# Kernel optimization log

Measured on AMD Instinct MI355X. Metric: run time of the kernel, lower is better.

## Reference

```python
import jax, jax.numpy as jnp
import numpy as np
import math

HIDDEN = 2048
NUM_HEADS = 16
HEAD_SIZE = HIDDEN // NUM_HEADS
BATCH = 2
SEQ = 2048


def setup_inputs() -> dict:
    key = jax.random.key(0)
    k_x, k_wq, k_bq, k_wo, k_bo = jax.random.split(key, 5)
    scale_in = 1.0 / math.sqrt(HIDDEN)
    return {
        "x": jax.random.normal(k_x, (BATCH, SEQ, HIDDEN), dtype=jnp.float32),
        # torch Linear stored as W[out,in]; we keep the jax-friendly transpose [in,out]
        "Wqkv": jax.random.normal(k_wq, (HIDDEN, 3 * HIDDEN), dtype=jnp.float32) * scale_in,
        "bqkv": jax.random.normal(k_bq, (3 * HIDDEN,), dtype=jnp.float32) * 0.01,
        "Wo": jax.random.normal(k_wo, (HIDDEN, HIDDEN), dtype=jnp.float32) * scale_in,
        "bo": jax.random.normal(k_bo, (HIDDEN,), dtype=jnp.float32) * 0.01,
    }


def reference(x, Wqkv, bqkv, Wo, bo):
    b, s, _ = x.shape
    # fused QKV projection; channel layout is (three, num_heads, head_size)
    kqv = x @ Wqkv + bqkv                      # [b, s, 3*hidden]
    kqv = kqv.reshape(b, s, 3, NUM_HEADS, HEAD_SIZE)
    q = kqv[:, :, 0]                           # [b, s, n, h]
    k = kqv[:, :, 1]
    v = kqv[:, :, 2]
    # scores[b, n, s_key, t_query] = K_s . Q_t, scaled
    scores = jnp.einsum('bsnh,btnh->bnst', k, q) / math.sqrt(HEAD_SIZE)
    # faithful to original: keep upper triangle (key <= query), masked entries are exactly -10000
    ones = jnp.ones_like(scores)
    scores = jnp.triu(scores) + (-10000.0) * jnp.tril(ones, k=-1)
    attn = jax.nn.softmax(scores, axis=2)      # softmax over key dim
    out = jnp.einsum('bnkq,bknh->bqnh', attn, v)  # [b, s, n, h]
    out = out.reshape(b, s, NUM_HEADS * HEAD_SIZE)
    return out @ Wo + bo
```

## Files before the change

kernel.cpp:

```cpp
#include <hip/hip_runtime.h>
#include <hip/hip_bf16.h>

typedef __hip_bfloat16 bf16;
typedef __attribute__((ext_vector_type(8))) short short8;
typedef __attribute__((ext_vector_type(8))) unsigned short ushort8;
typedef __attribute__((ext_vector_type(4))) float floatx4;

#define BATCH 2
#define S_LEN 2048
#define NHEAD 16
#define HD 128
#define HIDDEN 2048
#define QSCALE 0.12754435f
#define FOFF 12.0f

static __device__ __forceinline__ unsigned short f2bf(float f) {
    union { float f; unsigned int u; } c; c.f = f;
    unsigned int u = c.u;
    unsigned int rounded = u + 0x7FFF + ((u >> 16) & 1);
    return (unsigned short)(rounded >> 16);
}

__global__ __launch_bounds__(256) void cast_f32_bf16(const float* __restrict__ src,
                                                     bf16* __restrict__ dst) {
    int i = (blockIdx.x * 256 + threadIdx.x) * 8;
    float4 a = *(const float4*)&src[i];
    float4 b = *(const float4*)&src[i + 4];
    ushort8 o;
    o[0] = f2bf(a.x); o[1] = f2bf(a.y); o[2] = f2bf(a.z); o[3] = f2bf(a.w);
    o[4] = f2bf(b.x); o[5] = f2bf(b.y); o[6] = f2bf(b.z); o[7] = f2bf(b.w);
    *(ushort8*)&dst[i] = o;
}

__global__ __launch_bounds__(256) void cast_transpose(const float* __restrict__ src,
                                                      bf16* __restrict__ dst,
                                                      int R, int C) {
    __shared__ unsigned short t[32][33];
    int tx = threadIdx.x & 31, ty = threadIdx.x >> 5;
    int c0 = blockIdx.x * 32, r0 = blockIdx.y * 32;
#pragma unroll
    for (int i = 0; i < 4; i++) {
        int r = r0 + ty + i * 8;
        t[ty + i * 8][tx] = f2bf(src[(size_t)r * C + c0 + tx]);
    }
    __syncthreads();
#pragma unroll
    for (int i = 0; i < 4; i++) {
        int cc = c0 + ty + i * 8;
        ((unsigned short*)dst)[(size_t)cc * R + r0 + tx] = t[tx][ty + i * 8];
    }
}

#define GK 2048
#define NT 32

#define STGA(s, h)                                                              \
    __builtin_amdgcn_global_load_lds(                                           \
        (const __attribute__((address_space(1))) void*)(pA + (size_t)((h) * 64) * GK + (s) * 64), \
        (__attribute__((address_space(3))) void*)(lA + ((s) & 1) * 32768 + (h) * 8192 + ldst),    \
        16, 0, 0)
#define STGB(s, h)                                                              \
    __builtin_amdgcn_global_load_lds(                                           \
        (const __attribute__((address_space(1))) void*)(pB + (size_t)((h) * 64) * GK + (s) * 64), \
        (__attribute__((address_space(3))) void*)(lB + ((s) & 1) * 16384 + (h) * 8192 + ldst),    \
        16, 0, 0)

#define LDA(i, ks) (*(const short8*)(Ab + ((((wm * 64 + (i) * 16 + lr) << 7) + (ks) * 64 + quad * 16) ^ axor)))
#define LDB(j, ks) (*(const short8*)(Bb + ((((wn * 64 + (j) * 16 + lr) << 7) + (ks) * 64 + quad * 16) ^ axor)))

#define PH8(IOFF, BF, JOFF)                                                     \
    __builtin_amdgcn_s_setprio(1);                                              \
    _Pragma("unroll")                                                           \
    for (int ks = 0; ks < 2; ks++)                                              \
        _Pragma("unroll")                                                       \
        for (int ii = 0; ii < 2; ii++)                                          \
            _Pragma("unroll")                                                   \
            for (int jj = 0; jj < 2; jj++)                                      \
                acc[(IOFF) + ii][(JOFF) + jj] = __builtin_amdgcn_mfma_f32_16x16x32_bf16( \
                    aF[ii][ks], BF[jj][ks], acc[(IOFF) + ii][(JOFF) + jj], 0, 0, 0); \
    __builtin_amdgcn_s_setprio(0);

#define BAR __builtin_amdgcn_s_barrier()
#define LGKM0 asm volatile("s_waitcnt lgkmcnt(0)" ::: "memory")

template <int EPI>
__global__ __launch_bounds__(512, 2) void gemm256(const bf16* __restrict__ A,
                                                  const bf16* __restrict__ Bt,
                                                  const float* __restrict__ bias,
                                                  bf16* __restrict__ Qb,
                                                  bf16* __restrict__ Kb,
                                                  bf16* __restrict__ Vt,
                                                  float* __restrict__ Cout,
                                                  int ntN) {
    __shared__ __align__(16) bf16 Asm[2][256 * 64];
    __shared__ __align__(16) bf16 Bsm[2][128 * 64];

    int tid = threadIdx.x;
    int wave = tid >> 6, lane = tid & 63;
    int quad = lane >> 4, lr = lane & 15;
    int wm = wave >> 1, wn = wave & 1;
    int axor = (lr & 7) << 4;

    int nwg = gridDim.x;
    int cpx = nwg >> 3;
    int bid = blockIdx.x;
    int swz = (bid & 7) * cpx + (bid >> 3);
    int mt = swz / ntN, nt = swz - mt * ntN;
    int m0 = mt * 256, n0 = nt * 128;

    int srow = wave * 8 + (lane >> 3);
    int scol = ((lane & 7) ^ ((lane >> 3) & 7)) * 8;
    const bf16* pA = A + (size_t)(m0 + srow) * GK + scol;
    const bf16* pB = Bt + (size_t)(n0 + srow) * GK + scol;
    char* lA = (char*)&Asm[0][0];
    char* lB = (char*)&Bsm[0][0];
    int ldst = wave * 1024;

    const floatx4 fzero = {0.f, 0.f, 0.f, 0.f};
    floatx4 acc[4][4];
#pragma unroll
    for (int i = 0; i < 4; i++)
#pragma unroll
        for (int j = 0; j < 4; j++) acc[i][j] = fzero;

    short8 aF[2][2], b0F[2][2], b1F[2][2];

    STGB(0, 0); STGB(0, 1); STGA(0, 0); STGA(0, 1); STGA(0, 2); STGA(0, 3);
    STGB(1, 0); STGB(1, 1); STGA(1, 0); STGA(1, 1); STGA(1, 2); STGA(1, 3);
    asm volatile("s_waitcnt vmcnt(6)" ::: "memory");
    BAR;

    for (int t = 0; t < NT; ++t) {
        const char* Ab = lA + (t & 1) * 32768;
        const char* Bb = lB + (t & 1) * 16384;

#pragma unroll
        for (int ii = 0; ii < 2; ii++) { aF[ii][0] = LDA(ii, 0); aF[ii][1] = LDA(ii, 1); }
#pragma unroll
        for (int jj = 0; jj < 2; jj++) { b0F[jj][0] = LDB(jj, 0); b0F[jj][1] = LDB(jj, 1); }
        BAR; LGKM0;
        PH8(0, b0F, 0)
        BAR;

#pragma unroll
        for (int jj = 0; jj < 2; jj++) { b1F[jj][0] = LDB(jj + 2, 0); b1F[jj][1] = LDB(jj + 2, 1); }
        BAR; LGKM0;
        PH8(0, b1F, 2)
        BAR;

#pragma unroll
        for (int ii = 0; ii < 2; ii++) { aF[ii][0] = LDA(ii + 2, 0); aF[ii][1] = LDA(ii + 2, 1); }
        if (t + 2 < NT) { STGB(t + 2, 0); STGB(t + 2, 1); }
        BAR; LGKM0;
        PH8(2, b1F, 2)
        BAR;

        if (t + 2 < NT) {
            STGA(t + 2, 0); STGA(t + 2, 1); STGA(t + 2, 2); STGA(t + 2, 3);
            asm volatile("s_waitcnt vmcnt(6)" ::: "memory");
        } else {
            asm volatile("s_waitcnt vmcnt(0)" ::: "memory");
        }
        BAR;
        PH8(2, b0F, 0)
        BAR;
    }

    if (EPI == 0) {
#pragma unroll
        for (int i = 0; i < 4; i++) {
#pragma unroll
            for (int j = 0; j < 4; j++) {
                int gcn = n0 + wn * 64 + j * 16 + lr;
                float bv = bias[gcn];
                int tsel = gcn >> 11, hh = (gcn >> 7) & 15, d = gcn & 127;
#pragma unroll
                for (int reg = 0; reg < 4; reg++) {
                    int gm = m0 + wm * 64 + i * 16 + quad * 4 + reg;
                    float v = acc[i][j][reg] + bv;
                    int bb = gm >> 11, s = gm & 2047;
                    size_t hb = (size_t)(bb * NHEAD + hh);
                    if (tsel == 0) {
                        Qb[(hb * S_LEN + s) * HD + d] = __float2bfloat16(v * QSCALE);
                    } else if (tsel == 1) {
                        Kb[(hb * S_LEN + s) * HD + d] = __float2bfloat16(v);
                    } else {
                        Vt[(hb * HD + d) * S_LEN + s] = __float2bfloat16(v);
                    }
                }
            }
        }
    } else {
        int N = ntN << 7;
#pragma unroll
        for (int i = 0; i < 4; i++) {
#pragma unroll
            for (int j = 0; j < 4; j++) {
                int gcn = n0 + wn * 64 + j * 16 + lr;
                float bv = bias[gcn];
#pragma unroll
                for (int reg = 0; reg < 4; reg++) {
                    int gm = m0 + wm * 64 + i * 16 + quad * 4 + reg;
                    Cout[(size_t)gm * N + gcn] = acc[i][j][reg] + bv;
                }
            }
        }
    }
}

#define PSTR 72
__global__ __launch_bounds__(256, 2) void attn_kernel(const bf16* __restrict__ Qb,
                                                      const bf16* __restrict__ Kb,
                                                      const bf16* __restrict__ Vt,
                                                      bf16* __restrict__ Obuf) {
    __shared__ __align__(16) bf16 Ks[64 * 128];
    __shared__ __align__(16) bf16 Vs[128 * 64];
    __shared__ __align__(16) bf16 Ps[4][16 * PSTR];

    int tid = threadIdx.x;
    int wave = tid >> 6, lane = tid & 63;
    int quad = lane >> 4, lr = lane & 15;
    int srow = lane >> 4;
    int head = blockIdx.x, p = blockIdx.y, b = blockIdx.z;
    size_t hb = (size_t)(b * NHEAD + head);
    const bf16* Qbase = Qb + hb * S_LEN * HD;
    const bf16* Kbase = Kb + hb * S_LEN * HD;
    const bf16* Vbase = Vt + hb * (size_t)HD * S_LEN;

    const floatx4 fzero = {0.f, 0.f, 0.f, 0.f};
    const float MASKV = -30000.f;
    short8 ones;
#pragma unroll
    for (int i = 0; i < 8; i++) ones[i] = (short)0x3F80;

    for (int sub = 0; sub < 2; sub++) {
        int qt = sub ? (31 - p) : p;
        int q0 = qt * 64;
        int niter = qt + 1;

        short8 qF[4];
#pragma unroll
        for (int kc = 0; kc < 4; kc++)
            qF[kc] = *(const short8*)&Qbase[(size_t)(q0 + wave * 16 + lr) * HD + kc * 32 + quad * 8];

        floatx4 Oacc[8];
        floatx4 lacc = fzero;
#pragma unroll
        for (int dn = 0; dn < 8; dn++) Oacc[dn] = fzero;

        ushort8 kpre[4], vpre[4];
#pragma unroll
        for (int i = 0; i < 4; i++) {
            int rl = wave * 16 + i * 4 + srow;
            int gc = lr ^ (rl & 15);
            kpre[i] = *(const ushort8*)&Kbase[(size_t)rl * HD + gc * 8];
            int vr = wave * 32 + i * 8 + (lane >> 3);
            int gvc = (lane & 7) ^ (vr & 7);
            vpre[i] = *(const ushort8*)&Vbase[(size_t)vr * S_LEN + gvc * 8];
        }

        for (int kt = 0; kt < niter; kt++) {
            __syncthreads();
#pragma unroll
            for (int i = 0; i < 4; i++) {
                *(ushort8*)&Ks[(wave * 16 + i * 4) * 128 + lane * 8] = kpre[i];
                *(ushort8*)&Vs[(wave * 32 + i * 8) * 64 + lane * 8] = vpre[i];
            }
            __syncthreads();
            if (kt + 1 < niter) {
                int ns0 = (kt + 1) * 64;
#pragma unroll
                for (int i = 0; i < 4; i++) {
                    int rl = wave * 16 + i * 4 + srow;
                    int gc = lr ^ (rl & 15);
                    kpre[i] = *(const ushort8*)&Kbase[(size_t)(ns0 + rl) * HD + gc * 8];
                    int vr = wave * 32 + i * 8 + (lane >> 3);
                    int gvc = (lane & 7) ^ (vr & 7);
                    vpre[i] = *(const ushort8*)&Vbase[(size_t)vr * S_LEN + ns0 + gvc * 8];
                }
            }

            floatx4 sc[4];
#pragma unroll
            for (int nt = 0; nt < 4; nt++) sc[nt] = fzero;
#pragma unroll
            for (int kc = 0; kc < 4; kc++)
#pragma unroll
                for (int nt = 0; nt < 4; nt++) {
                    short8 kf = *(const short8*)&Ks[(nt * 16 + lr) * 128 + (((kc * 4 + quad) ^ lr) & 15) * 8];
                    sc[nt] = __builtin_amdgcn_mfma_f32_16x16x32_bf16(qF[kc], kf, sc[nt], 0, 0, 0);
                }
            if (kt == niter - 1) {
#pragma unroll
                for (int nt = 0; nt < 4; nt++)
#pragma unroll
                    for (int reg = 0; reg < 4; reg++) {
                        int qg = wave * 16 + quad * 4 + reg;
                        int kg = nt * 16 + lr;
                        if (kg > qg) sc[nt][reg] = MASKV;
                    }
            }
#pragma unroll
            for (int nt = 0; nt < 4; nt++)
#pragma unroll
                for (int reg = 0; reg < 4; reg++) {
                    float pv = __builtin_amdgcn_exp2f(sc[nt][reg] - FOFF);
                    Ps[wave][(quad * 4 + reg) * PSTR + nt * 16 + lr] = __float2bfloat16(pv);
                }
#pragma unroll
            for (int st = 0; st < 2; st++) {
                short8 aP = *(const short8*)&Ps[wave][lr * PSTR + st * 32 + quad * 8];
                lacc = __builtin_amdgcn_mfma_f32_16x16x32_bf16(aP, ones, lacc, 0, 0, 0);
#pragma unroll
                for (int dn = 0; dn < 8; dn++) {
                    short8 vf = *(const short8*)&Vs[(dn * 16 + lr) * 64 + (((st * 4 + quad) ^ (lr & 7)) & 7) * 8];
                    Oacc[dn] = __builtin_amdgcn_mfma_f32_16x16x32_bf16(aP, vf, Oacc[dn], 0, 0, 0);
                }
            }
        }

#pragma unroll
        for (int reg = 0; reg < 4; reg++) {
            float inv = 1.0f / lacc[reg];
            int qg = q0 + wave * 16 + quad * 4 + reg;
#pragma unroll
            for (int dn = 0; dn < 8; dn++) {
                int d = dn * 16 + lr;
                Obuf[((size_t)(b * S_LEN + qg)) * HIDDEN + head * HD + d] =
                    __float2bfloat16(Oacc[dn][reg] * inv);
            }
        }
    }
}

extern "C" void kernel_launch(void* const* d_in, const int* in_sizes, int n_in,
                              void* d_out, int out_size, void* d_ws, size_t ws_size,
                              hipStream_t stream) {
    (void)in_sizes; (void)n_in; (void)out_size; (void)ws_size;
    const float* x    = (const float*)d_in[0];
    const float* Wqkv = (const float*)d_in[1];
    const float* bqkv = (const float*)d_in[2];
    const float* Wo   = (const float*)d_in[3];
    const float* bo   = (const float*)d_in[4];
    float* out = (float*)d_out;

    bf16* ws = (bf16*)d_ws;
    bf16* Xb    = ws;
    bf16* Obuf  = ws;
    bf16* WqkvT = ws + (size_t)8388608;
    bf16* WoT   = WqkvT;
    bf16* Qb    = WqkvT + (size_t)12582912;
    bf16* Kb    = Qb + (size_t)8388608;
    bf16* Vt    = Kb + (size_t)8388608;

    cast_f32_bf16<<<4096, 256, 0, stream>>>(x, Xb);
    cast_transpose<<<dim3(192, 64), 256, 0, stream>>>(Wqkv, WqkvT, 2048, 6144);
    gemm256<0><<<dim3(768), dim3(512), 0, stream>>>(Xb, WqkvT, bqkv, Qb, Kb, Vt, nullptr, 48);
    cast_transpose<<<dim3(64, 64), 256, 0, stream>>>(Wo, WoT, 2048, 2048);
    attn_kernel<<<dim3(16, 16, 2), 256, 0, stream>>>(Qb, Kb, Vt, Obuf);
    gemm256<1><<<dim3(256), dim3(512), 0, stream>>>(Obuf, WoT, bo, nullptr, nullptr, nullptr, out, 16);
}
```

Measured before the change: 415.1 us.

## Replace 256x128 GEMM tile with 128x128 tile and simplified single-phase pipeline

The QKV and output projection GEMMs now use a 128x128 tile with 256 threads (4 waves) instead of a 256x128 tile with 512 threads, which doubles the grid size. The four-phase inner loop with many barriers becomes a single batch of LDS reads issued through inline ds_read_b128, split waits on lgkmcnt, and one barrier per k-step, with global-to-LDS prefetch issued after the MFMAs. The aim is fewer barriers, better overlap of LDS reads with MFMA work, and more workgroups to fill the GPU. The smaller tile lowers operand reuse and raises global/L2 traffic per FLOP.

```diff
diff --git a/kernel.cpp b/kernel.cpp
--- a/kernel.cpp
+++ b/kernel.cpp
@@ -19,6 +19,12 @@
     unsigned int u = c.u;
     unsigned int rounded = u + 0x7FFF + ((u >> 16) & 1);
     return (unsigned short)(rounded >> 16);
+}
+
+static __device__ __forceinline__ short8 lds_read16(unsigned off) {
+    short8 r;
+    asm volatile("ds_read_b128 %0, %1" : "=v"(r) : "v"(off));
+    return r;
 }
 
 __global__ __launch_bounds__(256) void cast_f32_bf16(const float* __restrict__ src,
@@ -54,37 +60,31 @@
 #define GK 2048
 #define NT 32
 
-#define STGA(s, h)                                                              \
-    __builtin_amdgcn_global_load_lds(                                           \
-        (const __attribute__((address_space(1))) void*)(pA + (size_t)((h) * 64) * GK + (s) * 64), \
-        (__attribute__((address_space(3))) void*)(lA + ((s) & 1) * 32768 + (h) * 8192 + ldst),    \
-        16, 0, 0)
-#define STGB(s, h)                                                              \
-    __builtin_amdgcn_global_load_lds(                                           \
-        (const __attribute__((address_space(1))) void*)(pB + (size_t)((h) * 64) * GK + (s) * 64), \
-        (__attribute__((address_space(3))) void*)(lB + ((s) & 1) * 16384 + (h) * 8192 + ldst),    \
-        16, 0, 0)
-
-#define LDA(i, ks) (*(const short8*)(Ab + ((((wm * 64 + (i) * 16 + lr) << 7) + (ks) * 64 + quad * 16) ^ axor)))
-#define LDB(j, ks) (*(const short8*)(Bb + ((((wn * 64 + (j) * 16 + lr) << 7) + (ks) * 64 + quad * 16) ^ axor)))
-
-#define PH8(IOFF, BF, JOFF)                                                     \
-    __builtin_amdgcn_s_setprio(1);                                              \
-    _Pragma("unroll")                                                           \
-    for (int ks = 0; ks < 2; ks++)                                              \
+#define BAR __builtin_amdgcn_s_barrier()
+#define SCHED0 __builtin_amdgcn_sched_barrier(0)
+
+static __device__ __forceinline__ void gll(const bf16* g, char* l) {
+    __builtin_amdgcn_global_load_lds(
+        (const __attribute__((address_space(1))) void*)g,
+        (__attribute__((address_space(3))) void*)l, 16, 0, 0);
+}
+
+#define STG8(s)                                                                 \
+    do {                                                                        \
         _Pragma("unroll")                                                       \
-        for (int ii = 0; ii < 2; ii++)                                          \
-            _Pragma("unroll")                                                   \
-            for (int jj = 0; jj < 2; jj++)                                      \
-                acc[(IOFF) + ii][(JOFF) + jj] = __builtin_amdgcn_mfma_f32_16x16x32_bf16( \
-                    aF[ii][ks], BF[jj][ks], acc[(IOFF) + ii][(JOFF) + jj], 0, 0, 0); \
-    __builtin_amdgcn_s_setprio(0);
-
-#define BAR __builtin_amdgcn_s_barrier()
-#define LGKM0 asm volatile("s_waitcnt lgkmcnt(0)" ::: "memory")
+        for (int ld = 0; ld < 4; ld++) {                                        \
+            gll(pA + (size_t)(ld * 8) * GK + (s) * 64,                          \
+                lA + ((s) & 1) * 16384 + wave * 4096 + ld * 1024);              \
+            gll(pB + (size_t)(ld * 8) * GK + (s) * 64,                          \
+                lB + ((s) & 1) * 16384 + wave * 4096 + ld * 1024);              \
+        }                                                                       \
+    } while (0)
+
+#define RD_A(i, ks) aF[i][ks] = lds_read16(Ab + ((unsigned)((wm * 64 + (i) * 16 + lr) << 7)) + ((unsigned)(((ks) * 64 + quad * 16)) ^ axor));
+#define RD_B(j, ks) bF[j][ks] = lds_read16(Bb + ((unsigned)((wn * 64 + (j) * 16 + lr) << 7)) + ((unsigned)(((ks) * 64 + quad * 16)) ^ axor));
 
 template <int EPI>
-__global__ __launch_bounds__(512, 2) void gemm256(const bf16* __restrict__ A,
+__global__ __launch_bounds__(256, 2) void gemm128(const bf16* __restrict__ A,
                                                   const bf16* __restrict__ Bt,
                                                   const float* __restrict__ bias,
                                                   bf16* __restrict__ Qb,
@@ -92,29 +92,31 @@
                                                   bf16* __restrict__ Vt,
                                                   float* __restrict__ Cout,
                                                   int ntN) {
-    __shared__ __align__(16) bf16 Asm[2][256 * 64];
+    __shared__ __align__(16) bf16 Asm[2][128 * 64];
     __shared__ __align__(16) bf16 Bsm[2][128 * 64];
 
     int tid = threadIdx.x;
     int wave = tid >> 6, lane = tid & 63;
     int quad = lane >> 4, lr = lane & 15;
     int wm = wave >> 1, wn = wave & 1;
-    int axor = (lr & 7) << 4;
+    unsigned axor = (unsigned)((lr & 7) << 4);
 
     int nwg = gridDim.x;
     int cpx = nwg >> 3;
     int bid = blockIdx.x;
     int swz = (bid & 7) * cpx + (bid >> 3);
     int mt = swz / ntN, nt = swz - mt * ntN;
-    int m0 = mt * 256, n0 = nt * 128;
-
-    int srow = wave * 8 + (lane >> 3);
+    int m0 = mt * 128, n0 = nt * 128;
+
+    int srow = wave * 32 + (lane >> 3);
     int scol = ((lane & 7) ^ ((lane >> 3) & 7)) * 8;
     const bf16* pA = A + (size_t)(m0 + srow) * GK + scol;
     const bf16* pB = Bt + (size_t)(n0 + srow) * GK + scol;
     char* lA = (char*)&Asm[0][0];
     char* lB = (char*)&Bsm[0][0];
-    int ldst = wave * 1024;
+
+    unsigned aBase0 = (unsigned)(size_t)(__attribute__((address_space(3))) char*)lA;
+    unsigned bBase0 = (unsigned)(size_t)(__attribute__((address_space(3))) char*)lB;
 
     const floatx4 fzero = {0.f, 0.f, 0.f, 0.f};
     floatx4 acc[4][4];
@@ -123,46 +125,57 @@
 #pragma unroll
         for (int j = 0; j < 4; j++) acc[i][j] = fzero;
 
-    short8 aF[2][2], b0F[2][2], b1F[2][2];
-
-    STGB(0, 0); STGB(0, 1); STGA(0, 0); STGA(0, 1); STGA(0, 2); STGA(0, 3);
-    STGB(1, 0); STGB(1, 1); STGA(1, 0); STGA(1, 1); STGA(1, 2); STGA(1, 3);
-    asm volatile("s_waitcnt vmcnt(6)" ::: "memory");
+    short8 aF[4][2], bF[4][2];
+
+    STG8(0);
+    STG8(1);
+    asm volatile("s_waitcnt vmcnt(8)" ::: "memory");
     BAR;
 
     for (int t = 0; t < NT; ++t) {
-        const char* Ab = lA + (t & 1) * 32768;
-        const char* Bb = lB + (t & 1) * 16384;
-
-#pragma unroll
-        for (int ii = 0; ii < 2; ii++) { aF[ii][0] = LDA(ii, 0); aF[ii][1] = LDA(ii, 1); }
-#pragma unroll
-        for (int jj = 0; jj < 2; jj++) { b0F[jj][0] = LDB(jj, 0); b0F[jj][1] = LDB(jj, 1); }
-        BAR; LGKM0;
-        PH8(0, b0F, 0)
+        unsigned Ab = aBase0 + (unsigned)((t & 1) * 16384);
+        unsigned Bb = bBase0 + (unsigned)((t & 1) * 16384);
+
+        RD_B(0, 0) RD_B(0, 1) RD_B(1, 0) RD_B(1, 1)
+        RD_A(0, 0) RD_A(0, 1) RD_A(1, 0) RD_A(1, 1)
+        RD_A(2, 0) RD_A(2, 1) RD_A(3, 0) RD_A(3, 1)
+        RD_B(2, 0) RD_B(2, 1) RD_B(3, 0) RD_B(3, 1)
+
+        asm volatile("s_waitcnt lgkmcnt(4)" ::: "memory");
+        SCHED0;
+        __builtin_amdgcn_s_setprio(1);
+#pragma unroll
+        for (int ks = 0; ks < 2; ks++)
+#pragma unroll
+            for (int i = 0; i < 4; i++)
+#pragma unroll
+                for (int j = 0; j < 2; j++)
+                    acc[i][j] = __builtin_amdgcn_mfma_f32_16x16x32_bf16(
+                        aF[i][ks], bF[j][ks], acc[i][j], 0, 0, 0);
+        __builtin_amdgcn_s_setprio(0);
+
+        asm volatile("s_waitcnt lgkmcnt(0)" ::: "memory");
+        SCHED0;
+        __builtin_amdgcn_s_setprio(1);
+#pragma unroll
+        for (int ks = 0; ks < 2; ks++)
+#pragma unroll
+            for (int i = 0; i < 4; i++)
+#pragma unroll
+                for (int j = 2; j < 4; j++)
+                    acc[i][j] = __builtin_amdgcn_mfma_f32_16x16x32_bf16(
+                        aF[i][ks], bF[j][ks], acc[i][j], 0, 0, 0);
+        __builtin_amdgcn_s_setprio(0);
+
         BAR;
-
-#pragma unroll
-        for (int jj = 0; jj < 2; jj++) { b1F[jj][0] = LDB(jj + 2, 0); b1F[jj][1] = LDB(jj + 2, 1); }
-        BAR; LGKM0;
-        PH8(0, b1F, 2)
-        BAR;
-
-#pragma unroll
-        for (int ii = 0; ii < 2; ii++) { aF[ii][0] = LDA(ii + 2, 0); aF[ii][1] = LDA(ii + 2, 1); }
-        if (t + 2 < NT) { STGB(t + 2, 0); STGB(t + 2, 1); }
-        BAR; LGKM0;
-        PH8(2, b1F, 2)
-        BAR;
-
+        SCHED0;
         if (t + 2 < NT) {
-            STGA(t + 2, 0); STGA(t + 2, 1); STGA(t + 2, 2); STGA(t + 2, 3);
-            asm volatile("s_waitcnt vmcnt(6)" ::: "memory");
+            STG8(t + 2);
+            SCHED0;
+            asm volatile("s_waitcnt vmcnt(8)" ::: "memory");
         } else {
             asm volatile("s_waitcnt vmcnt(0)" ::: "memory");
         }
-        BAR;
-        PH8(2, b0F, 0)
         BAR;
     }
 
@@ -355,8 +368,8 @@
 
     cast_f32_bf16<<<4096, 256, 0, stream>>>(x, Xb);
     cast_transpose<<<dim3(192, 64), 256, 0, stream>>>(Wqkv, WqkvT, 2048, 6144);
-    gemm256<0><<<dim3(768), dim3(512), 0, stream>>>(Xb, WqkvT, bqkv, Qb, Kb, Vt, nullptr, 48);
+    gemm128<0><<<dim3(1536), dim3(256), 0, stream>>>(Xb, WqkvT, bqkv, Qb, Kb, Vt, nullptr, 48);
     cast_transpose<<<dim3(64, 64), 256, 0, stream>>>(Wo, WoT, 2048, 2048);
     attn_kernel<<<dim3(16, 16, 2), 256, 0, stream>>>(Qb, Kb, Vt, Obuf);
-    gemm256<1><<<dim3(256), dim3(512), 0, stream>>>(Obuf, WoT, bo, nullptr, nullptr, nullptr, out, 16);
-}
+    gemm128<1><<<dim3(512), dim3(256), 0, stream>>>(Obuf, WoT, bo, nullptr, nullptr, nullptr, out, 16);
+}
```

Measured after the change: 371.8 us. 10.4% less time.
